# Kernel tuning notes

Measured on AMD Instinct MI355X. Metric: run time of the kernel, lower is better.

The kernel has to match this reference:

```python
import jax, jax.numpy as jnp
import numpy as np

HEAD, D_MODEL, D_KV, D_FF = 12, 768, 64, 3072
BS, S = 8, 512
D_K = D_MODEL // HEAD


def layer_norm(x, g, b, eps=1e-5):
    m = jnp.mean(x, axis=-1, keepdims=True)
    v = jnp.var(x, axis=-1, keepdims=True)
    return (x - m) / jnp.sqrt(v + eps) * g + b


def setup_inputs() -> dict:
    key = jax.random.key(0)
    ks = jax.random.split(key, 16)
    w = lambda k, *s: (jax.random.normal(k, s, dtype=jnp.float32) * 0.02)
    return {
        'x': jax.random.normal(ks[0], (BS, S, D_MODEL), dtype=jnp.float32),
        'pad_mask': jnp.ones((BS, S), dtype=bool),
        'prior': jnp.zeros((1, 1, 1, 1), dtype=jnp.float32),
        # GroupAttention params
        'ga_ln_g': jnp.ones((D_MODEL,), jnp.float32), 'ga_ln_b': jnp.zeros((D_MODEL,), jnp.float32),
        'ga_wq': w(ks[1], D_K, D_K), 'ga_bq': jnp.zeros((D_K,), jnp.float32),
        'ga_wk': w(ks[2], D_K, D_K), 'ga_bk': jnp.zeros((D_K,), jnp.float32),
        # ScaledDotProductAttention params (head*d_kv == d_model)
        'sa_wq': w(ks[3], HEAD * D_KV, D_MODEL), 'sa_bq': jnp.zeros((HEAD * D_KV,), jnp.float32),
        'sa_wk': w(ks[4], HEAD * D_KV, D_MODEL), 'sa_bk': jnp.zeros((HEAD * D_KV,), jnp.float32),
        'sa_wv': w(ks[5], HEAD * D_KV, D_MODEL), 'sa_bv': jnp.zeros((HEAD * D_KV,), jnp.float32),
        # FFN params
        'ff_w1': w(ks[6], D_FF, D_MODEL), 'ff_b1': jnp.zeros((D_FF,), jnp.float32),
        'ff_w2': w(ks[7], D_MODEL, D_FF), 'ff_b2': jnp.zeros((D_MODEL,), jnp.float32),
        # Sublayer (pre-)norms
        'sl0_g': jnp.ones((D_MODEL,), jnp.float32), 'sl0_b': jnp.zeros((D_MODEL,), jnp.float32),
        'sl1_g': jnp.ones((D_MODEL,), jnp.float32), 'sl1_b': jnp.zeros((D_MODEL,), jnp.float32),
    }


def group_attention(x, pad_mask, prior, ln_g, ln_b, wq, bq, wk, bk):
    bs, s = x.shape[:2]
    ctx = layer_norm(x, ln_g, ln_b).reshape(bs, s, HEAD, D_K).transpose(0, 2, 1, 3)  # [bs,h,s,dk]
    a = jnp.eye(s, k=1, dtype=jnp.float32)   # superdiag
    c = jnp.eye(s, k=-1, dtype=jnp.float32)  # subdiag
    diag = jnp.eye(s, dtype=bool)
    tridiag = (a + c) > 0
    mask = pad_mask[:, None, None, :] & tridiag[None, None]  # [bs,1,s,s]
    q = ctx @ wq.T + bq
    k = ctx @ wk.T + bk
    scores = jnp.einsum('bhqd,bhkd->bhqk', q, k) / D_K
    scores = jnp.where(mask, scores, -10000.0)
    na = jax.nn.softmax(scores, axis=-1)
    na = jnp.sqrt(na * na.swapaxes(-2, -1) + 1e-4)
    na = prior + (1.0 - prior) * na
    tri = jnp.triu(jnp.ones((s, s), jnp.float32))  # upper incl diag
    # keep log-values only on the superdiagonal, zero elsewhere
    t = jnp.where(a[None, None] > 0, jnp.log(na + 1e-9), 0.0) @ tri
    g = jnp.exp(tri @ t)
    # zero where tri - eye == 0 (diagonal and strict lower) -> keep strict upper
    g = jnp.where((tri - jnp.eye(s, dtype=jnp.float32))[None, None] == 0, 0.0, g)
    g_attn = g + g.swapaxes(-2, -1) + jnp.where(diag[None, None], na, 1e-4)
    return g_attn, na


def self_attention(xn, group_prob, wq, bq, wk, bk, wv, bv):
    bs, s = xn.shape[:2]
    q = (xn @ wq.T + bq).reshape(bs, s, HEAD, D_KV).transpose(0, 2, 1, 3)
    k = (xn @ wk.T + bk).reshape(bs, s, HEAD, D_KV).transpose(0, 2, 1, 3)
    v = (xn @ wv.T + bv).reshape(bs, s, HEAD, D_KV).transpose(0, 2, 1, 3)
    att = jnp.einsum('bhqd,bhkd->bhqk', q, k) / np.sqrt(D_KV).astype(np.float32)
    # NOTE: original uses non-inplace att.masked_fill(...) without assignment -> mask has no effect
    att = jax.nn.softmax(att, axis=-1) * group_prob
    out = jnp.einsum('bhqk,bhkd->bhqd', att, v)
    return out.transpose(0, 2, 1, 3).reshape(bs, s, HEAD * D_KV)


def reference(x, pad_mask, prior,
              ga_ln_g, ga_ln_b, ga_wq, ga_bq, ga_wk, ga_bk,
              sa_wq, sa_bq, sa_wk, sa_bk, sa_wv, sa_bv,
              ff_w1, ff_b1, ff_w2, ff_b2,
              sl0_g, sl0_b, sl1_g, sl1_b):
    group_prob, break_prob = group_attention(x, pad_mask, prior,
                                             ga_ln_g, ga_ln_b, ga_wq, ga_bq, ga_wk, ga_bk)
    # sublayer 0: pre-norm residual around self-attn weighted by group_prob
    x = x + self_attention(layer_norm(x, sl0_g, sl0_b), group_prob,
                           sa_wq, sa_bq, sa_wk, sa_bk, sa_wv, sa_bv)
    # sublayer 1: pre-norm residual around FFN
    h = jax.nn.relu(layer_norm(x, sl1_g, sl1_b) @ ff_w1.T + ff_b1)
    x = x + (h @ ff_w2.T + ff_b2)
    return (x, group_prob, break_prob)
```

## Files before the change

### kernel.cpp

```cpp
#include <hip/hip_runtime.h>
#include <hip/hip_bf16.h>

#define HEADS 12
#define DM    768
#define DKH   64
#define DFF   3072
#define BSZ   8
#define SEQ   512
#define MROWS (BSZ*SEQ)
#define BH    (BSZ*HEADS)

typedef __attribute__((ext_vector_type(8))) short bf16x8;
typedef __attribute__((ext_vector_type(4))) float f32x4;

__device__ __forceinline__ void gload_lds16(const ushort* g, ushort* l) {
  __builtin_amdgcn_global_load_lds(
      (const __attribute__((address_space(1))) unsigned int*)g,
      (__attribute__((address_space(3))) unsigned int*)l, 16, 0, 0);
}

__device__ __forceinline__ float b2f(ushort u) {
  union { unsigned int i; float f; } c; c.i = (unsigned int)u << 16; return c.f;
}

__device__ __forceinline__ void gb_rows_512(
    int row, int t, const float* __restrict__ nsWS, const float* __restrict__ cumWS,
    const float* __restrict__ prior, float* __restrict__ gp, float* __restrict__ bp) {
  int bh = row >> 9, q = row & 511;
  const float* cum = cumWS + (size_t)bh*SEQ;
  const float* ns  = nsWS  + (size_t)bh*SEQ;
  float pr = prior[0];
  float c0 = pr + (1.f - pr)*0.01f;
  float cq = cum[q];
  size_t rb = ((size_t)bh*SEQ + q)*SEQ;
  int k0 = (t & 127)*4;
  float4 g4, b4;
  float* gv = (float*)&g4; float* bv = (float*)&b4;
  #pragma unroll
  for (int j = 0; j < 4; ++j) {
    int k = k0 + j;
    float g;
    if (k == q) g = c0;
    else {
      float c = cum[k];
      g = __expf((k > q) ? (c - cq) : (cq - c)) + 1e-4f;
    }
    float bb = c0;
    if (k == q+1)      bb = ns[q];
    else if (k+1 == q) bb = ns[q-1];
    gv[j] = g; bv[j] = bb;
  }
  *(float4*)(gp + rb + k0) = g4;
  *(float4*)(bp + rb + k0) = b4;
}

__device__ __forceinline__ void gb_rows_256(
    int row, int t, const float* __restrict__ nsWS, const float* __restrict__ cumWS,
    const float* __restrict__ prior, float* __restrict__ gp, float* __restrict__ bp) {
  int bh = row >> 9, q = row & 511;
  const float* cum = cumWS + (size_t)bh*SEQ;
  const float* ns  = nsWS  + (size_t)bh*SEQ;
  float pr = prior[0];
  float c0 = pr + (1.f - pr)*0.01f;
  float cq = cum[q];
  size_t rb = ((size_t)bh*SEQ + q)*SEQ;
  int k0 = (t & 63)*8;
  float g8[8], b8[8];
  #pragma unroll
  for (int j = 0; j < 8; ++j) {
    int k = k0 + j;
    float g;
    if (k == q) g = c0;
    else {
      float c = cum[k];
      g = __expf((k > q) ? (c - cq) : (cq - c)) + 1e-4f;
    }
    float bb = c0;
    if (k == q+1)      bb = ns[q];
    else if (k+1 == q) bb = ns[q-1];
    g8[j] = g; b8[j] = bb;
  }
  *(float4*)(gp + rb + k0)     = *(float4*)&g8[0];
  *(float4*)(gp + rb + k0 + 4) = *(float4*)&g8[4];
  *(float4*)(bp + rb + k0)     = *(float4*)&b8[0];
  *(float4*)(bp + rb + k0 + 4) = *(float4*)&b8[4];
}

__global__ __launch_bounds__(256) void ln_cvt_kernel(
    const float* __restrict__ x,
    const float* __restrict__ g0, const float* __restrict__ b0, __hip_bfloat16* __restrict__ ln0,
    const float* __restrict__ gg, const float* __restrict__ gb, __hip_bfloat16* __restrict__ lnga,
    const float* __restrict__ swq, const float* __restrict__ swk, const float* __restrict__ swv,
    const float* __restrict__ w1s, const float* __restrict__ w2s,
    __hip_bfloat16* __restrict__ dqkv, __hip_bfloat16* __restrict__ d1,
    __hip_bfloat16* __restrict__ d2) {
  int t = threadIdx.x;
  if (blockIdx.x >= 1024) {
    long gid = (long)(blockIdx.x - 1024)*256 + t;
    long i = gid*4;
    const float* s; __hip_bfloat16* d; long off;
    if (i < 1769472L) {
      long j = i / 589824L; off = i - j*589824L;
      s = (j == 0) ? swq : (j == 1) ? swk : swv;
      d = dqkv + j*589824L;
    } else if (i < 4128768L) {
      off = i - 1769472L; s = w1s; d = d1;
    } else {
      off = i - 4128768L; s = w2s; d = d2;
    }
    float4 v = *(const float4*)(s + off);
    d[off+0] = __float2bfloat16(v.x);
    d[off+1] = __float2bfloat16(v.y);
    d[off+2] = __float2bfloat16(v.z);
    d[off+3] = __float2bfloat16(v.w);
    return;
  }
  int lane = t & 63, w = t >> 6;
  int row = blockIdx.x*4 + w;
  size_t base = (size_t)row * DM;
  float v[12]; float s = 0.f, s2 = 0.f;
  #pragma unroll
  for (int i = 0; i < 12; ++i) {
    v[i] = x[base + lane + 64*i];
    s += v[i]; s2 += v[i]*v[i];
  }
  #pragma unroll
  for (int off = 1; off < 64; off <<= 1) {
    s  += __shfl_xor(s,  off, 64);
    s2 += __shfl_xor(s2, off, 64);
  }
  float mean = s * (1.f/DM);
  float rstd = rsqrtf(s2 * (1.f/DM) - mean*mean + 1e-5f);
  #pragma unroll
  for (int i = 0; i < 12; ++i) {
    int c = lane + 64*i;
    float h = (v[i]-mean)*rstd;
    ln0[base + c]  = __float2bfloat16(h*g0[c] + b0[c]);
    lnga[base + c] = __float2bfloat16(h*gg[c] + gb[c]);
  }
}

__global__ __launch_bounds__(512) void ga_edges_kernel(
    const float* __restrict__ Qg, const float* __restrict__ Kg,
    const float* __restrict__ prior, float* __restrict__ nsWS, float* __restrict__ cumWS) {
  __shared__ float pu[SEQ], pd[SEQ];
  __shared__ float wsum[8], wpre[8];
  int bh = blockIdx.x, m = threadIdx.x;
  const float* Qb = Qg + (size_t)bh*SEQ*DKH;
  const float* Kb = Kg + (size_t)bh*SEQ*DKH;
  const float4* qm = (const float4*)(Qb + (size_t)m*DKH);
  float su = -1e4f, sd = -1e4f;
  if (m < SEQ-1) {
    const float4* kn = (const float4*)(Kb + (size_t)(m+1)*DKH);
    float a = 0.f;
    #pragma unroll
    for (int i = 0; i < 16; ++i) {
      float4 q4 = qm[i], k4 = kn[i];
      a += q4.x*k4.x + q4.y*k4.y + q4.z*k4.z + q4.w*k4.w;
    }
    su = a * (1.f/DKH);
  }
  if (m >= 1) {
    const float4* kp = (const float4*)(Kb + (size_t)(m-1)*DKH);
    float a = 0.f;
    #pragma unroll
    for (int i = 0; i < 16; ++i) {
      float4 q4 = qm[i], k4 = kp[i];
      a += q4.x*k4.x + q4.y*k4.y + q4.z*k4.z + q4.w*k4.w;
    }
    sd = a * (1.f/DKH);
  }
  float mx = fmaxf(su, sd);
  float eu = __expf(su - mx), ed = __expf(sd - mx);
  float inv = 1.f / (eu + ed);
  pu[m] = eu * inv;
  pd[m] = ed * inv;
  __syncthreads();
  float pr = prior[0];
  float nsv = 0.f, lg = 0.f;
  if (m < SEQ-1) {
    float vv = sqrtf(pu[m]*pd[m+1] + 1e-4f);
    nsv = pr + (1.f - pr)*vv;
    lg = __logf(nsv + 1e-9f);
  }
  float v = lg;
  #pragma unroll
  for (int off = 1; off < 64; off <<= 1) {
    float u = __shfl_up(v, off, 64);
    if ((m & 63) >= off) v += u;
  }
  if ((m & 63) == 63) wsum[m >> 6] = v;
  __syncthreads();
  if (m == 0) {
    float a = 0.f;
    #pragma unroll
    for (int i = 0; i < 8; ++i) { wpre[i] = a; a += wsum[i]; }
  }
  __syncthreads();
  float incl = v + wpre[m >> 6];
  nsWS[(size_t)bh*SEQ + m] = nsv;
  cumWS[(size_t)bh*SEQ + m] = incl - lg;
}

template<int MODE>
__global__ __launch_bounds__(512, 2) void gemm256_kernel(
    const __hip_bfloat16* __restrict__ A, const __hip_bfloat16* __restrict__ B,
    const float* __restrict__ b0, const float* __restrict__ b1, const float* __restrict__ b2,
    __hip_bfloat16* __restrict__ C, __hip_bfloat16* __restrict__ vT,
    const float* __restrict__ nsWS, const float* __restrict__ cumWS,
    const float* __restrict__ prior, float* __restrict__ gp, float* __restrict__ bp,
    const __hip_bfloat16* __restrict__ lnga,
    const float* __restrict__ gwq, const float* __restrict__ gbq,
    const float* __restrict__ gwk, const float* __restrict__ gbk,
    float* __restrict__ Qg, float* __restrict__ Kg) {
  constexpr int N    = (MODE==0) ? 2304 : (MODE==1) ? 3072 : 768;
  constexpr int TN   = N / 256;
  constexpr int LDAB = (MODE==2) ? 3072 : 768;
  constexpr int NT   = (MODE==0) ? 144 : (MODE==1) ? 192 : 192;
  __shared__ ushort LDS[65536];
  int t = threadIdx.x;
  int bidx = blockIdx.x;
  if (bidx >= NT) {
    if (MODE == 0) {
      ushort* WQ = LDS;
      ushort* WK = LDS + 4608;
      for (int i = t; i < 4096; i += 512) {
        int d = i >> 6, c = i & 63;
        __hip_bfloat16 q = __float2bfloat16(gwq[i]);
        __hip_bfloat16 k = __float2bfloat16(gwk[i]);
        WQ[d*72 + c] = *(ushort*)&q;
        WK[d*72 + c] = *(ushort*)&k;
      }
      __syncthreads();
      int task = (bidx - 144)*2 + (t >> 8);
      int h  = task >> 4;
      int r0 = (task & 15) * 256;
      int t2 = t & 255;
      int lane = t2 & 63, w = t2 >> 6;
      int lrow = lane & 15, lhi = lane >> 4;
      const ushort* Ag2 = (const ushort*)lnga;
      bf16x8 a[4][2];
      #pragma unroll
      for (int i = 0; i < 4; ++i)
        #pragma unroll
        for (int ks = 0; ks < 2; ++ks)
          a[i][ks] = *(const bf16x8*)(Ag2 + (size_t)(r0 + w*64 + i*16 + lrow)*DM + h*64 + ks*32 + lhi*8);
      int b = r0 >> 9;
      #pragma unroll
      for (int qk = 0; qk < 2; ++qk) {
        const ushort* Wm = qk ? WK : WQ;
        const float* bias = qk ? gbk : gbq;
        float* Og = qk ? Kg : Qg;
        bf16x8 bf[4][2];
        #pragma unroll
        for (int j = 0; j < 4; ++j)
          #pragma unroll
          for (int ks = 0; ks < 2; ++ks)
            bf[j][ks] = *(const bf16x8*)&Wm[(j*16 + lrow)*72 + ks*32 + lhi*8];
        f32x4 acc[4][4] = {};
        #pragma unroll
        for (int i = 0; i < 4; ++i)
          #pragma unroll
          for (int j = 0; j < 4; ++j) {
            acc[i][j] = __builtin_amdgcn_mfma_f32_16x16x32_bf16(a[i][0], bf[j][0], acc[i][j], 0, 0, 0);
            acc[i][j] = __builtin_amdgcn_mfma_f32_16x16x32_bf16(a[i][1], bf[j][1], acc[i][j], 0, 0, 0);
          }
        #pragma unroll
        for (int i = 0; i < 4; ++i) {
          int rowb = r0 + w*64 + i*16 + lhi*4;
          #pragma unroll
          for (int j = 0; j < 4; ++j) {
            int d = j*16 + lrow;
            float bv = bias[d];
            #pragma unroll
            for (int r = 0; r < 4; ++r) {
              int sIdx = (rowb + r) & 511;
              Og[(((size_t)b*HEADS + h)*SEQ + sIdx)*DKH + d] = acc[i][j][r] + bv;
            }
          }
        }
      }
    } else {
      int base = (MODE == 1) ? 16384 : 32768;
      int row = base + (bidx - NT)*4 + (t >> 7);
      gb_rows_512(row, t, nsWS, cumWS, prior, gp, bp);
    }
    return;
  }
  int lane = t & 63, w = t >> 6;
  int rin = lane >> 3, gr = lane & 7;
  int lrow = lane & 15, lhi = lane >> 4;
  int z = 0, tl = bidx;
  if (MODE == 2) { z = bidx / 48; tl = bidx % 48; }
  constexpr int NTIL = (MODE==2) ? 48 : NT;
  int tile = (tl & 7)*(NTIL/8) + (tl >> 3);
  int m0 = (tile / TN) * 256;
  int n0 = (tile % TN) * 256;
  int kOff = (MODE == 2) ? z * 768 : 0;
  if (MODE == 2) C += (size_t)z * MROWS * 768;
  int wr = w >> 2, wc = w & 3;
  const ushort* Ag = (const ushort*)A;
  const ushort* Bg = (const ushort*)B;
  f32x4 acc[8][4] = {};
  auto STAGE = [&](int p, int kt) {
    int k0 = kOff + kt*64;
    ushort* Ad = &LDS[p*16384];
    ushort* Bd = &LDS[32768 + p*16384];
    int cs = (gr ^ rin) * 8;
    #pragma unroll
    for (int q = 0; q < 4; ++q) {
      int rr = q*64 + w*8 + rin;
      gload_lds16(Ag + (size_t)(m0 + rr)*LDAB + k0 + cs, &Ad[(q*64 + w*8)*64]);
      gload_lds16(Bg + (size_t)(n0 + rr)*LDAB + k0 + cs, &Bd[(q*64 + w*8)*64]);
    }
  };
  const int nt = 12;
  STAGE(0, 0);
  STAGE(1, 1);
  asm volatile("s_waitcnt vmcnt(8)" ::: "memory");
  __builtin_amdgcn_s_barrier();
  int p = 0;
  for (int kt = 0; kt < nt; ++kt) {
    const ushort* Ar = &LDS[p*16384];
    const ushort* Br = &LDS[32768 + p*16384];
    int sw0 = (lhi ^ (lrow & 7)) * 8;
    int sw1 = ((4 + lhi) ^ (lrow & 7)) * 8;
    bf16x8 a0[8], b0r[4], a1[8], b1r[4];
    #pragma unroll
    for (int i = 0; i < 8; ++i)
      a0[i] = *(const bf16x8*)&Ar[(wr*128 + i*16 + lrow)*64 + sw0];
    #pragma unroll
    for (int j = 0; j < 4; ++j)
      b0r[j] = *(const bf16x8*)&Br[(wc*64 + j*16 + lrow)*64 + sw0];
    #pragma unroll
    for (int i = 0; i < 8; ++i)
      #pragma unroll
      for (int j = 0; j < 4; ++j)
        acc[i][j] = __builtin_amdgcn_mfma_f32_16x16x32_bf16(a0[i], b0r[j], acc[i][j], 0, 0, 0);
    #pragma unroll
    for (int i = 0; i < 8; ++i)
      a1[i] = *(const bf16x8*)&Ar[(wr*128 + i*16 + lrow)*64 + sw1];
    #pragma unroll
    for (int j = 0; j < 4; ++j)
      b1r[j] = *(const bf16x8*)&Br[(wc*64 + j*16 + lrow)*64 + sw1];
    asm volatile("s_waitcnt lgkmcnt(0)" ::: "memory");
    __builtin_amdgcn_sched_barrier(0);
    __builtin_amdgcn_s_barrier();
    if (kt + 2 < nt) STAGE(p, kt + 2);
    __builtin_amdgcn_s_setprio(1);
    #pragma unroll
    for (int i = 0; i < 8; ++i)
      #pragma unroll
      for (int j = 0; j < 4; ++j)
        acc[i][j] = __builtin_amdgcn_mfma_f32_16x16x32_bf16(a1[i], b1r[j], acc[i][j], 0, 0, 0);
    __builtin_amdgcn_s_setprio(0);
    if (kt + 1 < nt) {
      if (kt + 2 < nt) asm volatile("s_waitcnt vmcnt(8)" ::: "memory");
      else             asm volatile("s_waitcnt vmcnt(0)" ::: "memory");
      __builtin_amdgcn_s_barrier();
    }
    p ^= 1;
  }
  if (MODE == 0 && n0 >= 1536) {
    ushort* T = LDS;
    int b = m0 >> 9, s0 = m0 & 511;
    #pragma unroll
    for (int ps = 0; ps < 2; ++ps) {
      if ((wc >> 1) == ps) {
        #pragma unroll
        for (int j = 0; j < 4; ++j) {
          int dl = (wc & 1)*64 + j*16 + lrow;
          float bvv = b2[n0 - 1536 + ps*128 + dl];
          #pragma unroll
          for (int i = 0; i < 8; ++i) {
            #pragma unroll
            for (int r = 0; r < 4; ++r) {
              __hip_bfloat16 hh = __float2bfloat16(acc[i][j][r] + bvv);
              T[dl*264 + wr*128 + i*16 + lhi*4 + r] = *(ushort*)&hh;
            }
          }
        }
      }
      __syncthreads();
      #pragma unroll
      for (int it = 0; it < 8; ++it) {
        int idx = t + 512*it;
        int dl = idx >> 5, sc8 = (idx & 31)*8;
        int dg = n0 - 1536 + ps*128 + dl;
        int h = dg >> 6, dmod = dg & 63;
        bf16x8 vv = *(const bf16x8*)&T[dl*264 + sc8];
        *(bf16x8*)((ushort*)vT + ((size_t)(b*HEADS + h)*64 + dmod)*512 + s0 + sc8) = vv;
      }
      __syncthreads();
    }
    return;
  }
  #pragma unroll
  for (int i = 0; i < 8; ++i) {
    int grow = m0 + wr*128 + i*16 + lhi*4;
    #pragma unroll
    for (int j = 0; j < 4; ++j) {
      int gcol = n0 + wc*64 + j*16 + lrow;
      float bvv;
      if (MODE == 0)      bvv = (gcol < 768) ? b0[gcol] : b1[gcol-768];
      else if (MODE == 1) bvv = b0[gcol];
      else                bvv = 0.f;
      #pragma unroll
      for (int r = 0; r < 4; ++r) {
        float v = acc[i][j][r] + bvv;
        if (MODE == 1) v = fmaxf(v, 0.f);
        C[(size_t)(grow + r)*N + gcol] = __float2bfloat16(v);
      }
    }
  }
}

__global__ __launch_bounds__(256) void ffn2_reduce_kernel(
    const __hip_bfloat16* __restrict__ p, const float* __restrict__ bias,
    float* __restrict__ out) {
  int gid = blockIdx.x*256 + threadIdx.x;
  size_t i = (size_t)gid*8;
  const ushort* pp = (const ushort*)p;
  float acc[8];
  int col = (int)(i % DM);
  #pragma unroll
  for (int j = 0; j < 8; ++j) acc[j] = bias[col + j];
  #pragma unroll
  for (int s = 0; s < 4; ++s) {
    bf16x8 v = *(const bf16x8*)(pp + (size_t)s*MROWS*DM + i);
    #pragma unroll
    for (int j = 0; j < 8; ++j) acc[j] += b2f((ushort)v[j]);
  }
  float4 o0 = *(const float4*)(out + i);
  float4 o1 = *(const float4*)(out + i + 4);
  o0.x += acc[0]; o0.y += acc[1]; o0.z += acc[2]; o0.w += acc[3];
  o1.x += acc[4]; o1.y += acc[5]; o1.z += acc[6]; o1.w += acc[7];
  *(float4*)(out + i)     = o0;
  *(float4*)(out + i + 4) = o1;
}

__global__ __launch_bounds__(256) void ln_res_kernel(
    const float* __restrict__ x, const __hip_bfloat16* __restrict__ a, float* __restrict__ xs,
    const float* __restrict__ g, const float* __restrict__ b, __hip_bfloat16* __restrict__ o) {
  int t = threadIdx.x;
  int lane = t & 63, w = t >> 6;
  int row = blockIdx.x*4 + w;
  size_t base = (size_t)row * DM;
  const ushort* ab = (const ushort*)a;
  float v[12]; float s = 0.f, s2 = 0.f;
  #pragma unroll
  for (int i = 0; i < 12; ++i) {
    int c = lane + 64*i;
    v[i] = x[base + c] + b2f(ab[base + c]);
    xs[base + c] = v[i];
    s += v[i]; s2 += v[i]*v[i];
  }
  #pragma unroll
  for (int off = 1; off < 64; off <<= 1) {
    s  += __shfl_xor(s,  off, 64);
    s2 += __shfl_xor(s2, off, 64);
  }
  float mean = s * (1.f/DM);
  float rstd = rsqrtf(s2 * (1.f/DM) - mean*mean + 1e-5f);
  #pragma unroll
  for (int i = 0; i < 12; ++i) {
    int c = lane + 64*i;
    o[base + c] = __float2bfloat16((v[i]-mean)*rstd*g[c] + b[c]);
  }
}

__global__ __launch_bounds__(256) void attn_mfma_kernel(
    const __hip_bfloat16* __restrict__ qk, const __hip_bfloat16* __restrict__ vT,
    const float* __restrict__ cumWS, const float* __restrict__ prior,
    __hip_bfloat16* __restrict__ att,
    const float* __restrict__ nsWS, float* __restrict__ gp, float* __restrict__ bp) {
  __shared__ ushort Ps[4][16][72];
  int t = threadIdx.x;
  int bidx = blockIdx.x;
  if (bidx >= 768) {
    int row = (bidx - 768)*4 + (t >> 6);
    gb_rows_256(row, t, nsWS, cumWS, prior, gp, bp);
    return;
  }
  int lane = t & 63, wid = t >> 6;
  int tile = (bidx & 7)*96 + (bidx >> 3);
  int qt = tile & 7, bh = tile >> 3;
  int b = bh / HEADS, h = bh % HEADS;
  int lrow = lane & 15, lhi = lane >> 4;
  int qbase = qt*64 + wid*16;
  const ushort* qg = (const ushort*)qk;
  bf16x8 aq[2];
  {
    const ushort* qp = qg + (size_t)(b*SEQ + qbase + lrow)*2304 + h*64 + lhi*8;
    aq[0] = *(const bf16x8*)qp;
    aq[1] = *(const bf16x8*)(qp + 32);
  }
  const float* cum = cumWS + (size_t)bh*SEQ;
  float pr = prior[0];
  float c0 = pr + (1.f - pr)*0.01f;
  int qrow[4]; float cq[4];
  #pragma unroll
  for (int r = 0; r < 4; ++r) { qrow[r] = qbase + lhi*4 + r; cq[r] = cum[qrow[r]]; }
  float lsum[4] = {0.f, 0.f, 0.f, 0.f};
  f32x4 oacc[4] = {};
  const ushort* kg = qg + 768;
  const ushort* vg = (const ushort*)vT;
  for (int kt = 0; kt < 8; ++kt) {
    f32x4 sacc[4] = {};
    #pragma unroll
    for (int j = 0; j < 4; ++j) {
      const ushort* kp = kg + (size_t)(b*SEQ + kt*64 + j*16 + lrow)*2304 + h*64 + lhi*8;
      bf16x8 bk0 = *(const bf16x8*)kp;
      bf16x8 bk1 = *(const bf16x8*)(kp + 32);
      sacc[j] = __builtin_amdgcn_mfma_f32_16x16x32_bf16(aq[0], bk0, sacc[j], 0, 0, 0);
      sacc[j] = __builtin_amdgcn_mfma_f32_16x16x32_bf16(aq[1], bk1, sacc[j], 0, 0, 0);
    }
    float ck[4];
    #pragma unroll
    for (int j = 0; j < 4; ++j) ck[j] = cum[kt*64 + j*16 + lrow];
    #pragma unroll
    for (int j = 0; j < 4; ++j) {
      int kk = kt*64 + j*16 + lrow;
      #pragma unroll
      for (int r = 0; r < 4; ++r) {
        float e = __expf(fminf(sacc[j][r]*0.125f - 16.f, 60.f));
        lsum[r] += e;
        float dd = ck[j] - cq[r];
        float gpv = (kk == qrow[r]) ? c0 : (__expf((kk > qrow[r]) ? dd : -dd) + 1e-4f);
        __hip_bfloat16 pb = __float2bfloat16(e * gpv);
        Ps[wid][lhi*4 + r][j*16 + lrow] = *(ushort*)&pb;
      }
    }
    asm volatile("s_waitcnt lgkmcnt(0)" ::: "memory");
    #pragma unroll
    for (int c = 0; c < 2; ++c) {
      bf16x8 ap = *(const bf16x8*)&Ps[wid][lrow][c*32 + lhi*8];
      #pragma unroll
      for (int dj = 0; dj < 4; ++dj) {
        const ushort* vp = vg + ((size_t)bh*64 + dj*16 + lrow)*512 + kt*64 + c*32 + lhi*8;
        bf16x8 bv = *(const bf16x8*)vp;
        oacc[dj] = __builtin_amdgcn_mfma_f32_16x16x32_bf16(ap, bv, oacc[dj], 0, 0, 0);
      }
    }
  }
  #pragma unroll
  for (int off = 1; off < 16; off <<= 1) {
    #pragma unroll
    for (int r = 0; r < 4; ++r) lsum[r] += __shfl_xor(lsum[r], off, 64);
  }
  float inv[4];
  #pragma unroll
  for (int r = 0; r < 4; ++r) inv[r] = 1.f / lsum[r];
  #pragma unroll
  for (int dj = 0; dj < 4; ++dj) {
    #pragma unroll
    for (int r = 0; r < 4; ++r) {
      float v = oacc[dj][r] * inv[r];
      att[(size_t)(b*SEQ + qbase + lhi*4 + r)*DM + h*64 + dj*16 + lrow] = __float2bfloat16(v);
    }
  }
}

extern "C" void kernel_launch(void* const* d_in, const int* in_sizes, int n_in,
                              void* d_out, int out_size, void* d_ws, size_t ws_size,
                              hipStream_t stream) {
  const float* x      = (const float*)d_in[0];
  const float* prior  = (const float*)d_in[2];
  const float* ga_g   = (const float*)d_in[3];
  const float* ga_b   = (const float*)d_in[4];
  const float* ga_wq  = (const float*)d_in[5];
  const float* ga_bq  = (const float*)d_in[6];
  const float* ga_wk  = (const float*)d_in[7];
  const float* ga_bk  = (const float*)d_in[8];
  const float* sa_wq  = (const float*)d_in[9];
  const float* sa_bq  = (const float*)d_in[10];
  const float* sa_wk  = (const float*)d_in[11];
  const float* sa_bk  = (const float*)d_in[12];
  const float* sa_wv  = (const float*)d_in[13];
  const float* sa_bv  = (const float*)d_in[14];
  const float* ff_w1  = (const float*)d_in[15];
  const float* ff_b1  = (const float*)d_in[16];
  const float* ff_w2  = (const float*)d_in[17];
  const float* ff_b2  = (const float*)d_in[18];
  const float* sl0_g  = (const float*)d_in[19];
  const float* sl0_b  = (const float*)d_in[20];
  const float* sl1_g  = (const float*)d_in[21];
  const float* sl1_b  = (const float*)d_in[22];

  float* out_x  = (float*)d_out;
  float* out_gp = out_x  + (size_t)MROWS*DM;
  float* out_bp = out_gp + (size_t)BH*SEQ*SEQ;

  char* W = (char*)d_ws;
  __hip_bfloat16* ln0    = (__hip_bfloat16*)(W + 0);
  __hip_bfloat16* lnga   = (__hip_bfloat16*)(W + 6291456);
  float* Qg   = (float*)(W + 12582912);
  float* Kg   = (float*)(W + 25165824);
  __hip_bfloat16* qkv3   = (__hip_bfloat16*)(W + 37748736);
  __hip_bfloat16* vT     = (__hip_bfloat16*)(W + 56623104);
  __hip_bfloat16* attbuf = (__hip_bfloat16*)(W + 62914560);
  __hip_bfloat16* ln1    = (__hip_bfloat16*)(W + 69206016);
  __hip_bfloat16* wqkv   = (__hip_bfloat16*)(W + 75497472);
  __hip_bfloat16* w1     = (__hip_bfloat16*)(W + 79036416);
  __hip_bfloat16* w2     = (__hip_bfloat16*)(W + 83755008);
  __hip_bfloat16* hbuf   = (__hip_bfloat16*)(W + 88473600);
  __hip_bfloat16* parts  = (__hip_bfloat16*)(W + 113639424);
  float* nsWS  = (float*)(W + 138805248);
  float* cumWS = (float*)(W + 139001856);

  ln_cvt_kernel<<<7360, 256, 0, stream>>>(
      x, sl0_g, sl0_b, ln0, ga_g, ga_b, lnga,
      sa_wq, sa_wk, sa_wv, ff_w1, ff_w2, wqkv, w1, w2);
  gemm256_kernel<0><<<240, 512, 0, stream>>>(
      ln0, wqkv, sa_bq, sa_bk, sa_bv, qkv3, vT,
      nullptr, nullptr, nullptr, nullptr, nullptr,
      lnga, ga_wq, ga_bq, ga_wk, ga_bk, Qg, Kg);
  ga_edges_kernel<<<BH, SEQ, 0, stream>>>(Qg, Kg, prior, nsWS, cumWS);
  attn_mfma_kernel<<<768 + 4096, 256, 0, stream>>>(
      qkv3, vT, cumWS, prior, attbuf, nsWS, out_gp, out_bp);
  ln_res_kernel<<<1024, 256, 0, stream>>>(x, attbuf, out_x, sl1_g, sl1_b, ln1);
  gemm256_kernel<1><<<192 + 4096, 512, 0, stream>>>(
      ln1, w1, ff_b1, nullptr, nullptr, hbuf, nullptr,
      nsWS, cumWS, prior, out_gp, out_bp,
      nullptr, nullptr, nullptr, nullptr, nullptr, nullptr, nullptr);
  gemm256_kernel<2><<<192 + 4096, 512, 0, stream>>>(
      hbuf, w2, nullptr, nullptr, nullptr, parts, nullptr,
      nsWS, cumWS, prior, out_gp, out_bp,
      nullptr, nullptr, nullptr, nullptr, nullptr, nullptr, nullptr);
  ffn2_reduce_kernel<<<1536, 256, 0, stream>>>(parts, ff_b2, out_x);
}
```

Measured before the change: 235.9 us.

## Rebalance group/break prob writes and fuse split-K reduction into FFN2 GEMM

Moves the group_prob/break_prob row generation out of the two FFN GEMM launches and puts it into the attention kernel (more extra blocks) and the ln_res kernel. The separate ffn2 reduce kernel is replaced by a last-block-arrives reduction inside the split-K GEMM, using an atomic counter per tile and a memset of the counters. It also raises wave priority around the attention P·V MFMAs. The aim is to cut a kernel launch and keep the GEMMs from competing with bandwidth-heavy output writes. In exchange it adds an atomic/fence dependency and serial tail work in the last-arriving block.

```diff
diff --git a/kernel.cpp b/kernel.cpp
--- a/kernel.cpp
+++ b/kernel.cpp
@@ -21,37 +21,6 @@
 
 __device__ __forceinline__ float b2f(ushort u) {
   union { unsigned int i; float f; } c; c.i = (unsigned int)u << 16; return c.f;
-}
-
-__device__ __forceinline__ void gb_rows_512(
-    int row, int t, const float* __restrict__ nsWS, const float* __restrict__ cumWS,
-    const float* __restrict__ prior, float* __restrict__ gp, float* __restrict__ bp) {
-  int bh = row >> 9, q = row & 511;
-  const float* cum = cumWS + (size_t)bh*SEQ;
-  const float* ns  = nsWS  + (size_t)bh*SEQ;
-  float pr = prior[0];
-  float c0 = pr + (1.f - pr)*0.01f;
-  float cq = cum[q];
-  size_t rb = ((size_t)bh*SEQ + q)*SEQ;
-  int k0 = (t & 127)*4;
-  float4 g4, b4;
-  float* gv = (float*)&g4; float* bv = (float*)&b4;
-  #pragma unroll
-  for (int j = 0; j < 4; ++j) {
-    int k = k0 + j;
-    float g;
-    if (k == q) g = c0;
-    else {
-      float c = cum[k];
-      g = __expf((k > q) ? (c - cq) : (cq - c)) + 1e-4f;
-    }
-    float bb = c0;
-    if (k == q+1)      bb = ns[q];
-    else if (k+1 == q) bb = ns[q-1];
-    gv[j] = g; bv[j] = bb;
-  }
-  *(float4*)(gp + rb + k0) = g4;
-  *(float4*)(bp + rb + k0) = b4;
 }
 
 __device__ __forceinline__ void gb_rows_256(
@@ -207,8 +176,7 @@
     const __hip_bfloat16* __restrict__ A, const __hip_bfloat16* __restrict__ B,
     const float* __restrict__ b0, const float* __restrict__ b1, const float* __restrict__ b2,
     __hip_bfloat16* __restrict__ C, __hip_bfloat16* __restrict__ vT,
-    const float* __restrict__ nsWS, const float* __restrict__ cumWS,
-    const float* __restrict__ prior, float* __restrict__ gp, float* __restrict__ bp,
+    float* __restrict__ gp, int* __restrict__ cnt,
     const __hip_bfloat16* __restrict__ lnga,
     const float* __restrict__ gwq, const float* __restrict__ gbq,
     const float* __restrict__ gwk, const float* __restrict__ gbk,
@@ -216,74 +184,68 @@
   constexpr int N    = (MODE==0) ? 2304 : (MODE==1) ? 3072 : 768;
   constexpr int TN   = N / 256;
   constexpr int LDAB = (MODE==2) ? 3072 : 768;
-  constexpr int NT   = (MODE==0) ? 144 : (MODE==1) ? 192 : 192;
+  constexpr int NT   = (MODE==0) ? 144 : 192;
   __shared__ ushort LDS[65536];
   int t = threadIdx.x;
   int bidx = blockIdx.x;
-  if (bidx >= NT) {
-    if (MODE == 0) {
-      ushort* WQ = LDS;
-      ushort* WK = LDS + 4608;
-      for (int i = t; i < 4096; i += 512) {
-        int d = i >> 6, c = i & 63;
-        __hip_bfloat16 q = __float2bfloat16(gwq[i]);
-        __hip_bfloat16 k = __float2bfloat16(gwk[i]);
-        WQ[d*72 + c] = *(ushort*)&q;
-        WK[d*72 + c] = *(ushort*)&k;
-      }
-      __syncthreads();
-      int task = (bidx - 144)*2 + (t >> 8);
-      int h  = task >> 4;
-      int r0 = (task & 15) * 256;
-      int t2 = t & 255;
-      int lane = t2 & 63, w = t2 >> 6;
-      int lrow = lane & 15, lhi = lane >> 4;
-      const ushort* Ag2 = (const ushort*)lnga;
-      bf16x8 a[4][2];
+  if (MODE == 0 && bidx >= NT) {
+    ushort* WQ = LDS;
+    ushort* WK = LDS + 4608;
+    for (int i = t; i < 4096; i += 512) {
+      int d = i >> 6, c = i & 63;
+      __hip_bfloat16 q = __float2bfloat16(gwq[i]);
+      __hip_bfloat16 k = __float2bfloat16(gwk[i]);
+      WQ[d*72 + c] = *(ushort*)&q;
+      WK[d*72 + c] = *(ushort*)&k;
+    }
+    __syncthreads();
+    int task = (bidx - 144)*2 + (t >> 8);
+    int h  = task >> 4;
+    int r0 = (task & 15) * 256;
+    int t2 = t & 255;
+    int lane = t2 & 63, w = t2 >> 6;
+    int lrow = lane & 15, lhi = lane >> 4;
+    const ushort* Ag2 = (const ushort*)lnga;
+    bf16x8 a[4][2];
+    #pragma unroll
+    for (int i = 0; i < 4; ++i)
+      #pragma unroll
+      for (int ks = 0; ks < 2; ++ks)
+        a[i][ks] = *(const bf16x8*)(Ag2 + (size_t)(r0 + w*64 + i*16 + lrow)*DM + h*64 + ks*32 + lhi*8);
+    int b = r0 >> 9;
+    #pragma unroll
+    for (int qk = 0; qk < 2; ++qk) {
+      const ushort* Wm = qk ? WK : WQ;
+      const float* bias = qk ? gbk : gbq;
+      float* Og = qk ? Kg : Qg;
+      bf16x8 bf[4][2];
+      #pragma unroll
+      for (int j = 0; j < 4; ++j)
+        #pragma unroll
+        for (int ks = 0; ks < 2; ++ks)
+          bf[j][ks] = *(const bf16x8*)&Wm[(j*16 + lrow)*72 + ks*32 + lhi*8];
+      f32x4 acc[4][4] = {};
       #pragma unroll
       for (int i = 0; i < 4; ++i)
         #pragma unroll
-        for (int ks = 0; ks < 2; ++ks)
-          a[i][ks] = *(const bf16x8*)(Ag2 + (size_t)(r0 + w*64 + i*16 + lrow)*DM + h*64 + ks*32 + lhi*8);
-      int b = r0 >> 9;
-      #pragma unroll
-      for (int qk = 0; qk < 2; ++qk) {
-        const ushort* Wm = qk ? WK : WQ;
-        const float* bias = qk ? gbk : gbq;
-        float* Og = qk ? Kg : Qg;
-        bf16x8 bf[4][2];
+        for (int j = 0; j < 4; ++j) {
+          acc[i][j] = __builtin_amdgcn_mfma_f32_16x16x32_bf16(a[i][0], bf[j][0], acc[i][j], 0, 0, 0);
+          acc[i][j] = __builtin_amdgcn_mfma_f32_16x16x32_bf16(a[i][1], bf[j][1], acc[i][j], 0, 0, 0);
+        }
+      #pragma unroll
+      for (int i = 0; i < 4; ++i) {
+        int rowb = r0 + w*64 + i*16 + lhi*4;
         #pragma unroll
-        for (int j = 0; j < 4; ++j)
+        for (int j = 0; j < 4; ++j) {
+          int d = j*16 + lrow;
+          float bv = bias[d];
           #pragma unroll
-          for (int ks = 0; ks < 2; ++ks)
-            bf[j][ks] = *(const bf16x8*)&Wm[(j*16 + lrow)*72 + ks*32 + lhi*8];
-        f32x4 acc[4][4] = {};
-        #pragma unroll
-        for (int i = 0; i < 4; ++i)
-          #pragma unroll
-          for (int j = 0; j < 4; ++j) {
-            acc[i][j] = __builtin_amdgcn_mfma_f32_16x16x32_bf16(a[i][0], bf[j][0], acc[i][j], 0, 0, 0);
-            acc[i][j] = __builtin_amdgcn_mfma_f32_16x16x32_bf16(a[i][1], bf[j][1], acc[i][j], 0, 0, 0);
-          }
-        #pragma unroll
-        for (int i = 0; i < 4; ++i) {
-          int rowb = r0 + w*64 + i*16 + lhi*4;
-          #pragma unroll
-          for (int j = 0; j < 4; ++j) {
-            int d = j*16 + lrow;
-            float bv = bias[d];
-            #pragma unroll
-            for (int r = 0; r < 4; ++r) {
-              int sIdx = (rowb + r) & 511;
-              Og[(((size_t)b*HEADS + h)*SEQ + sIdx)*DKH + d] = acc[i][j][r] + bv;
-            }
+          for (int r = 0; r < 4; ++r) {
+            int sIdx = (rowb + r) & 511;
+            Og[(((size_t)b*HEADS + h)*SEQ + sIdx)*DKH + d] = acc[i][j][r] + bv;
           }
         }
       }
-    } else {
-      int base = (MODE == 1) ? 16384 : 32768;
-      int row = base + (bidx - NT)*4 + (t >> 7);
-      gb_rows_512(row, t, nsWS, cumWS, prior, gp, bp);
     }
     return;
   }
@@ -297,6 +259,7 @@
   int m0 = (tile / TN) * 256;
   int n0 = (tile % TN) * 256;
   int kOff = (MODE == 2) ? z * 768 : 0;
+  __hip_bfloat16* Cbase = C;
   if (MODE == 2) C += (size_t)z * MROWS * 768;
   int wr = w >> 2, wc = w & 3;
   const ushort* Ag = (const ushort*)A;
@@ -413,36 +376,52 @@
       }
     }
   }
-}
-
-__global__ __launch_bounds__(256) void ffn2_reduce_kernel(
-    const __hip_bfloat16* __restrict__ p, const float* __restrict__ bias,
-    float* __restrict__ out) {
-  int gid = blockIdx.x*256 + threadIdx.x;
-  size_t i = (size_t)gid*8;
-  const ushort* pp = (const ushort*)p;
-  float acc[8];
-  int col = (int)(i % DM);
-  #pragma unroll
-  for (int j = 0; j < 8; ++j) acc[j] = bias[col + j];
-  #pragma unroll
-  for (int s = 0; s < 4; ++s) {
-    bf16x8 v = *(const bf16x8*)(pp + (size_t)s*MROWS*DM + i);
-    #pragma unroll
-    for (int j = 0; j < 8; ++j) acc[j] += b2f((ushort)v[j]);
-  }
-  float4 o0 = *(const float4*)(out + i);
-  float4 o1 = *(const float4*)(out + i + 4);
-  o0.x += acc[0]; o0.y += acc[1]; o0.z += acc[2]; o0.w += acc[3];
-  o1.x += acc[4]; o1.y += acc[5]; o1.z += acc[6]; o1.w += acc[7];
-  *(float4*)(out + i)     = o0;
-  *(float4*)(out + i + 4) = o1;
+  if (MODE == 2) {
+    __shared__ int lastFlag;
+    __threadfence();
+    __syncthreads();
+    if (t == 0) lastFlag = (atomicAdd(&cnt[tl], 1) == 3) ? 1 : 0;
+    __syncthreads();
+    if (lastFlag) {
+      __threadfence();
+      const ushort* pp = (const ushort*)Cbase;
+      #pragma unroll
+      for (int it = 0; it < 16; ++it) {
+        int idx = it*512 + t;
+        int rr = idx >> 5;
+        int cc = (idx & 31) * 8;
+        size_t gof = (size_t)(m0 + rr)*768 + n0 + cc;
+        float a8[8];
+        #pragma unroll
+        for (int j = 0; j < 8; ++j) a8[j] = b0[n0 + cc + j];
+        #pragma unroll
+        for (int z2 = 0; z2 < 4; ++z2) {
+          bf16x8 v = *(const bf16x8*)(pp + (size_t)z2*MROWS*768 + gof);
+          #pragma unroll
+          for (int j = 0; j < 8; ++j) a8[j] += b2f((ushort)v[j]);
+        }
+        float4 o0 = *(const float4*)(gp + gof);
+        float4 o1 = *(const float4*)(gp + gof + 4);
+        o0.x += a8[0]; o0.y += a8[1]; o0.z += a8[2]; o0.w += a8[3];
+        o1.x += a8[4]; o1.y += a8[5]; o1.z += a8[6]; o1.w += a8[7];
+        *(float4*)(gp + gof)     = o0;
+        *(float4*)(gp + gof + 4) = o1;
+      }
+    }
+  }
 }
 
 __global__ __launch_bounds__(256) void ln_res_kernel(
     const float* __restrict__ x, const __hip_bfloat16* __restrict__ a, float* __restrict__ xs,
-    const float* __restrict__ g, const float* __restrict__ b, __hip_bfloat16* __restrict__ o) {
+    const float* __restrict__ g, const float* __restrict__ b, __hip_bfloat16* __restrict__ o,
+    const float* __restrict__ nsWS, const float* __restrict__ cumWS,
+    const float* __restrict__ prior, float* __restrict__ gp, float* __restrict__ bp) {
   int t = threadIdx.x;
+  if (blockIdx.x >= 1024) {
+    int row = 32768 + (blockIdx.x - 1024)*4 + (t >> 6);
+    gb_rows_256(row, t, nsWS, cumWS, prior, gp, bp);
+    return;
+  }
   int lane = t & 63, w = t >> 6;
   int row = blockIdx.x*4 + w;
   size_t base = (size_t)row * DM;
@@ -532,6 +511,7 @@
       }
     }
     asm volatile("s_waitcnt lgkmcnt(0)" ::: "memory");
+    __builtin_amdgcn_s_setprio(1);
     #pragma unroll
     for (int c = 0; c < 2; ++c) {
       bf16x8 ap = *(const bf16x8*)&Ps[wid][lrow][c*32 + lhi*8];
@@ -542,6 +522,7 @@
         oacc[dj] = __builtin_amdgcn_mfma_f32_16x16x32_bf16(ap, bv, oacc[dj], 0, 0, 0);
       }
     }
+    __builtin_amdgcn_s_setprio(0);
   }
   #pragma unroll
   for (int off = 1; off < 16; off <<= 1) {
@@ -607,25 +588,25 @@
   __hip_bfloat16* parts  = (__hip_bfloat16*)(W + 113639424);
   float* nsWS  = (float*)(W + 138805248);
   float* cumWS = (float*)(W + 139001856);
-
+  int*   cnt   = (int*)  (W + 139198464);
+
+  hipMemsetAsync(cnt, 0, 48*sizeof(int), stream);
   ln_cvt_kernel<<<7360, 256, 0, stream>>>(
       x, sl0_g, sl0_b, ln0, ga_g, ga_b, lnga,
       sa_wq, sa_wk, sa_wv, ff_w1, ff_w2, wqkv, w1, w2);
   gemm256_kernel<0><<<240, 512, 0, stream>>>(
-      ln0, wqkv, sa_bq, sa_bk, sa_bv, qkv3, vT,
-      nullptr, nullptr, nullptr, nullptr, nullptr,
+      ln0, wqkv, sa_bq, sa_bk, sa_bv, qkv3, vT, nullptr, nullptr,
       lnga, ga_wq, ga_bq, ga_wk, ga_bk, Qg, Kg);
   ga_edges_kernel<<<BH, SEQ, 0, stream>>>(Qg, Kg, prior, nsWS, cumWS);
-  attn_mfma_kernel<<<768 + 4096, 256, 0, stream>>>(
+  attn_mfma_kernel<<<768 + 8192, 256, 0, stream>>>(
       qkv3, vT, cumWS, prior, attbuf, nsWS, out_gp, out_bp);
-  ln_res_kernel<<<1024, 256, 0, stream>>>(x, attbuf, out_x, sl1_g, sl1_b, ln1);
-  gemm256_kernel<1><<<192 + 4096, 512, 0, stream>>>(
-      ln1, w1, ff_b1, nullptr, nullptr, hbuf, nullptr,
-      nsWS, cumWS, prior, out_gp, out_bp,
+  ln_res_kernel<<<1024 + 4096, 256, 0, stream>>>(
+      x, attbuf, out_x, sl1_g, sl1_b, ln1,
+      nsWS, cumWS, prior, out_gp, out_bp);
+  gemm256_kernel<1><<<192, 512, 0, stream>>>(
+      ln1, w1, ff_b1, nullptr, nullptr, hbuf, nullptr, nullptr, nullptr,
       nullptr, nullptr, nullptr, nullptr, nullptr, nullptr, nullptr);
-  gemm256_kernel<2><<<192 + 4096, 512, 0, stream>>>(
-      hbuf, w2, nullptr, nullptr, nullptr, parts, nullptr,
-      nsWS, cumWS, prior, out_gp, out_bp,
+  gemm256_kernel<2><<<192, 512, 0, stream>>>(
+      hbuf, w2, ff_b2, nullptr, nullptr, parts, nullptr, out_x, cnt,
       nullptr, nullptr, nullptr, nullptr, nullptr, nullptr, nullptr);
-  ffn2_reduce_kernel<<<1536, 256, 0, stream>>>(parts, ff_b2, out_x);
-}
+}
```

After: 331.6 us. +40.6%, slower.
